# Performance work log

Measured on AMD Instinct MI355X. Metric: run time of the kernel, lower is better.

Reference implementation:

```python
import jax, jax.numpy as jnp
import numpy as np


def dequantize_sparse_sinq(W_q, scales, zeros, mask, scale2, group_size):
    """SINQ-style dual-scaled grouped dequant with sparsity mask.

    W = ((W_q - zeros) * scales) broadcast over groups along the in-dim,
    then scaled per input column by scale2, then masked (pruned weights -> 0).
    W_q: [O, I] int; scales/zeros: [O, I//g]; scale2: [I]; mask: [O, I] bool.
    """
    O, I = W_q.shape
    g = group_size
    Wq = W_q.astype(jnp.float32).reshape(O, I // g, g)
    W = (Wq - zeros[:, :, None]) * scales[:, :, None]  # grouped affine dequant
    W = W.reshape(O, I) * scale2[None, :]              # second (column) scale
    return jnp.where(mask, W, jnp.zeros((), dtype=W.dtype))


def setup_inputs() -> dict:
    key = jax.random.key(0)
    ks = jax.random.split(key, 7)
    B, S, I, O, G = 8, 2048, 4096, 4096, 128
    x = jax.random.normal(ks[0], (B, S, I), dtype=jnp.float32)
    W_q = jax.random.randint(ks[1], (O, I), 0, 16, dtype=jnp.int32)
    scales = jax.random.uniform(ks[2], (O, I // G), dtype=jnp.float32)
    zeros = jax.random.uniform(ks[3], (O, I // G), dtype=jnp.float32)
    mask = jax.random.randint(ks[4], (O, I), 0, 2, dtype=jnp.int32).astype(jnp.bool_)
    scale2 = jax.random.uniform(ks[5], (I,), dtype=jnp.float32)
    bias = jax.random.normal(ks[6], (O,), dtype=jnp.float32)
    return {"x": x, "W_q": W_q, "scales": scales, "zeros": zeros,
            "mask": mask, "scale2": scale2, "bias": bias, "group_size": G}


def reference(x, W_q, scales, zeros, mask, scale2, bias, group_size):
    W = dequantize_sparse_sinq(W_q, scales, zeros, mask, scale2, group_size)
    W = W.astype(x.dtype)
    out = jnp.einsum('bsi,oi->bso', x, W)  # matmul(x, W.T)
    out = out + bias
    return out
```

## Files before the change

### kernel.cpp

```cpp
#include <hip/hip_runtime.h>
#include <hip/hip_bf16.h>
#include <stdint.h>


typedef short s16x8 __attribute__((ext_vector_type(8)));
typedef short s16x4 __attribute__((ext_vector_type(4)));
typedef float f32x4 __attribute__((ext_vector_type(4)));

#define BM 128
#define BN 128
#define BK 64
#define LDSS 72

static __device__ __forceinline__ short f2bf(float f) {
    __hip_bfloat16 h = __float2bfloat16(f);
    return *reinterpret_cast<short*>(&h);
}

__global__ __launch_bounds__(256)
void dequant_kernel(const int* __restrict__ Wq,
                    const float* __restrict__ scales,
                    const float* __restrict__ zeros,
                    const void* __restrict__ mask_raw,
                    const float* __restrict__ scale2,
                    short* __restrict__ Wb,
                    int O, int I, int G) {
    __shared__ int lds_flag;
    if (threadIdx.x == 0) lds_flag = 0;
    __syncthreads();
    {
        unsigned v = ((const unsigned*)mask_raw)[threadIdx.x & 255];
        if (v > 1u) lds_flag = 1;
    }
    __syncthreads();
    const bool mask_is_byte = (lds_flag != 0);

    long long idx = ((long long)blockIdx.x * 256 + threadIdx.x) * 8;
    if (idx >= (long long)O * I) return;
    int o = (int)(idx / I);
    int i = (int)(idx % I);
    int gi = o * (I / G) + i / G;
    float s = scales[gi];
    float z = zeros[gi];

    int4 w0 = *(const int4*)(Wq + idx);
    int4 w1 = *(const int4*)(Wq + idx + 4);
    float4 s2a = *(const float4*)(scale2 + i);
    float4 s2b = *(const float4*)(scale2 + i + 4);

    unsigned m[8];
    if (mask_is_byte) {
        unsigned long long mb = *(const unsigned long long*)((const unsigned char*)mask_raw + idx);
        #pragma unroll
        for (int j = 0; j < 8; ++j) m[j] = (unsigned)((mb >> (8 * j)) & 0xffULL);
    } else {
        int4 ma = *(const int4*)((const int*)mask_raw + idx);
        int4 mbv = *(const int4*)((const int*)mask_raw + idx + 4);
        m[0] = ma.x;  m[1] = ma.y;  m[2] = ma.z;  m[3] = ma.w;
        m[4] = mbv.x; m[5] = mbv.y; m[6] = mbv.z; m[7] = mbv.w;
    }

    float v[8];
    v[0] = ((float)w0.x - z) * s * s2a.x;
    v[1] = ((float)w0.y - z) * s * s2a.y;
    v[2] = ((float)w0.z - z) * s * s2a.z;
    v[3] = ((float)w0.w - z) * s * s2a.w;
    v[4] = ((float)w1.x - z) * s * s2b.x;
    v[5] = ((float)w1.y - z) * s * s2b.y;
    v[6] = ((float)w1.z - z) * s * s2b.z;
    v[7] = ((float)w1.w - z) * s * s2b.w;

    union { s16x8 v; int4 q; } out;
    #pragma unroll
    for (int j = 0; j < 8; ++j) {
        float masked = m[j] ? v[j] : 0.0f;
        out.v[j] = f2bf(masked);
    }
    *(int4*)(Wb + idx) = out.q;
}

__global__ __launch_bounds__(256, 2)
void gemm_kernel(const float* __restrict__ X,
                 const short* __restrict__ Wb,
                 const float* __restrict__ bias,
                 float* __restrict__ Out,
                 int M, int N, int K) {
    __shared__ short As[BM * LDSS];
    __shared__ short Bs[BN * LDSS];

    const int tid  = threadIdx.x;
    const int m0   = blockIdx.y * BM;
    const int n0   = blockIdx.x * BN;
    const int wave = tid >> 6;
    const int lane = tid & 63;
    const int wm   = (wave >> 1) * 64;
    const int wn   = (wave & 1) * 64;
    const int lr   = lane & 15;
    const int lq   = lane >> 4;

    f32x4 acc[4][4] = {};

    for (int k0 = 0; k0 < K; k0 += BK) {
        #pragma unroll
        for (int t = 0; t < 8; ++t) {
            int c   = tid + t * 256;
            int row = c >> 4;
            int col = (c & 15) * 4;
            float4 xv = *(const float4*)(X + (size_t)(m0 + row) * K + k0 + col);
            s16x4 bv;
            bv[0] = f2bf(xv.x); bv[1] = f2bf(xv.y);
            bv[2] = f2bf(xv.z); bv[3] = f2bf(xv.w);
            *(s16x4*)&As[row * LDSS + col] = bv;
        }
        #pragma unroll
        for (int t = 0; t < 4; ++t) {
            int c   = tid + t * 256;
            int row = c >> 3;
            int col = (c & 7) * 8;
            s16x8 wv = *(const s16x8*)(Wb + (size_t)(n0 + row) * K + k0 + col);
            *(s16x8*)&Bs[row * LDSS + col] = wv;
        }
        __syncthreads();

        #pragma unroll
        for (int kk = 0; kk < BK; kk += 32) {
            s16x8 af[4], bf[4];
            #pragma unroll
            for (int mi = 0; mi < 4; ++mi)
                af[mi] = *(const s16x8*)&As[(wm + mi * 16 + lr) * LDSS + kk + lq * 8];
            #pragma unroll
            for (int ni = 0; ni < 4; ++ni)
                bf[ni] = *(const s16x8*)&Bs[(wn + ni * 16 + lr) * LDSS + kk + lq * 8];
            #pragma unroll
            for (int mi = 0; mi < 4; ++mi)
                #pragma unroll
                for (int ni = 0; ni < 4; ++ni)
                    acc[mi][ni] = __builtin_amdgcn_mfma_f32_16x16x32_bf16(
                        af[mi], bf[ni], acc[mi][ni], 0, 0, 0);
        }
        __syncthreads();
    }

    #pragma unroll
    for (int ni = 0; ni < 4; ++ni) {
        int nc = n0 + wn + ni * 16 + lr;
        float bv = bias[nc];
        #pragma unroll
        for (int mi = 0; mi < 4; ++mi) {
            int mr = m0 + wm + mi * 16 + lq * 4;
            #pragma unroll
            for (int r = 0; r < 4; ++r)
                Out[(size_t)(mr + r) * N + nc] = acc[mi][ni][r] + bv;
        }
    }
}

extern "C" void kernel_launch(void* const* d_in, const int* in_sizes, int n_in,
                              void* d_out, int out_size, void* d_ws, size_t ws_size,
                              hipStream_t stream) {
    const float* x      = (const float*)d_in[0];
    const int*   Wq     = (const int*)d_in[1];
    const float* scales = (const float*)d_in[2];
    const float* zeros  = (const float*)d_in[3];
    const void*  mask   = (const void*)d_in[4];
    const float* scale2 = (const float*)d_in[5];
    const float* bias   = (const float*)d_in[6];
    float*       out    = (float*)d_out;

    const int I = in_sizes[5];
    const int O = in_sizes[6];
    const int M = (int)(in_sizes[0] / I);
    const int G = (int)(((long long)O * I) / in_sizes[2]);

    short* Wb = (short*)d_ws;

    long long total = (long long)O * I;
    int dq_blocks = (int)((total / 8 + 255) / 256);
    dequant_kernel<<<dq_blocks, 256, 0, stream>>>(Wq, scales, zeros, mask,
                                                  scale2, Wb, O, I, G);

    dim3 grid(O / BN, M / BM);
    gemm_kernel<<<grid, 256, 0, stream>>>(x, Wb, bias, out, M, O, I);
}
```

Before: 1.161 ms.

## Pre-convert activations to bf16 and stream GEMM tiles directly into LDS

Adds a separate kernel that converts X from fp32 to bf16 in workspace. A new GEMM then loads both bf16 operands straight from global memory into LDS with global_load_lds, avoiding per-tile conversion and register staging. It also switches the dequant indexing to 32-bit arithmetic. The cost is an extra full pass over X: an fp32 read plus a bf16 write. The unpadded 64-wide LDS rows may also cause bank conflicts during fragment reads. The new path runs only when the workspace is large enough.

```diff
diff --git a/kernel.cpp b/kernel.cpp
--- a/kernel.cpp
+++ b/kernel.cpp
@@ -35,10 +35,10 @@
     __syncthreads();
     const bool mask_is_byte = (lds_flag != 0);
 
-    long long idx = ((long long)blockIdx.x * 256 + threadIdx.x) * 8;
-    if (idx >= (long long)O * I) return;
-    int o = (int)(idx / I);
-    int i = (int)(idx % I);
+    int idx = (blockIdx.x * 256 + threadIdx.x) * 8;
+    if (idx >= O * I) return;
+    int o = idx / I;
+    int i = idx - o * I;
     int gi = o * (I / G) + i / G;
     float s = scales[gi];
     float z = zeros[gi];
@@ -77,6 +77,90 @@
         out.v[j] = f2bf(masked);
     }
     *(int4*)(Wb + idx) = out.q;
+}
+
+__global__ __launch_bounds__(256)
+void convert_x_kernel(const float* __restrict__ X, short* __restrict__ Xb, int n8) {
+    int c = blockIdx.x * 256 + threadIdx.x;
+    if (c >= n8) return;
+    size_t idx = (size_t)c * 8;
+    float4 a = *(const float4*)(X + idx);
+    float4 b = *(const float4*)(X + idx + 4);
+    union { s16x8 v; int4 q; } o;
+    o.v[0] = f2bf(a.x); o.v[1] = f2bf(a.y); o.v[2] = f2bf(a.z); o.v[3] = f2bf(a.w);
+    o.v[4] = f2bf(b.x); o.v[5] = f2bf(b.y); o.v[6] = f2bf(b.z); o.v[7] = f2bf(b.w);
+    *(int4*)(Xb + idx) = o.q;
+}
+
+__global__ __launch_bounds__(256, 2)
+void gemm_bb_kernel(const short* __restrict__ Xb,
+                    const short* __restrict__ Wb,
+                    const float* __restrict__ bias,
+                    float* __restrict__ Out,
+                    int M, int N, int K) {
+    __shared__ short As[BM * BK];
+    __shared__ short Bs[BN * BK];
+
+    const int tid  = threadIdx.x;
+    const int m0   = blockIdx.y * BM;
+    const int n0   = blockIdx.x * BN;
+    const int wave = tid >> 6;
+    const int lane = tid & 63;
+    const int wm   = (wave >> 1) * 64;
+    const int wn   = (wave & 1) * 64;
+    const int lr   = lane & 15;
+    const int lq   = lane >> 4;
+
+    f32x4 acc[4][4] = {};
+
+    const short* gA = Xb + (size_t)(m0 + (tid >> 3)) * K + (tid & 7) * 8;
+    const short* gB = Wb + (size_t)(n0 + (tid >> 3)) * K + (tid & 7) * 8;
+    short* lA = &As[wave * 512];
+    short* lB = &Bs[wave * 512];
+
+    for (int k0 = 0; k0 < K; k0 += BK) {
+        #pragma unroll
+        for (int t = 0; t < 4; ++t) {
+            __builtin_amdgcn_global_load_lds(
+                (const __attribute__((address_space(1))) void*)(gA + (size_t)t * 32 * K + k0),
+                (__attribute__((address_space(3))) void*)(lA + t * 2048), 16, 0, 0);
+            __builtin_amdgcn_global_load_lds(
+                (const __attribute__((address_space(1))) void*)(gB + (size_t)t * 32 * K + k0),
+                (__attribute__((address_space(3))) void*)(lB + t * 2048), 16, 0, 0);
+        }
+        __syncthreads();
+
+        #pragma unroll
+        for (int kk = 0; kk < BK; kk += 32) {
+            s16x8 af[4], bfv[4];
+            #pragma unroll
+            for (int mi = 0; mi < 4; ++mi)
+                af[mi] = *(const s16x8*)&As[(wm + mi * 16 + lr) * BK + kk + lq * 8];
+            #pragma unroll
+            for (int ni = 0; ni < 4; ++ni)
+                bfv[ni] = *(const s16x8*)&Bs[(wn + ni * 16 + lr) * BK + kk + lq * 8];
+            #pragma unroll
+            for (int mi = 0; mi < 4; ++mi)
+                #pragma unroll
+                for (int ni = 0; ni < 4; ++ni)
+                    acc[mi][ni] = __builtin_amdgcn_mfma_f32_16x16x32_bf16(
+                        af[mi], bfv[ni], acc[mi][ni], 0, 0, 0);
+        }
+        __syncthreads();
+    }
+
+    #pragma unroll
+    for (int ni = 0; ni < 4; ++ni) {
+        int nc = n0 + wn + ni * 16 + lr;
+        float bv = bias[nc];
+        #pragma unroll
+        for (int mi = 0; mi < 4; ++mi) {
+            int mr = m0 + wm + mi * 16 + lq * 4;
+            #pragma unroll
+            for (int r = 0; r < 4; ++r)
+                Out[(size_t)(mr + r) * N + nc] = acc[mi][ni][r] + bv;
+        }
+    }
 }
 
 __global__ __launch_bounds__(256, 2)
@@ -173,12 +257,22 @@
     const int G = (int)(((long long)O * I) / in_sizes[2]);
 
     short* Wb = (short*)d_ws;
-
-    long long total = (long long)O * I;
-    int dq_blocks = (int)((total / 8 + 255) / 256);
+    size_t wbBytes = (size_t)O * I * sizeof(short);
+    size_t xbBytes = (size_t)M * I * sizeof(short);
+
+    long long totalW = (long long)O * I;
+    int dq_blocks = (int)((totalW / 8 + 255) / 256);
     dequant_kernel<<<dq_blocks, 256, 0, stream>>>(Wq, scales, zeros, mask,
                                                   scale2, Wb, O, I, G);
 
     dim3 grid(O / BN, M / BM);
-    gemm_kernel<<<grid, 256, 0, stream>>>(x, Wb, bias, out, M, O, I);
-}
+    if (ws_size >= wbBytes + xbBytes) {
+        short* Xb = (short*)((char*)d_ws + wbBytes);
+        int n8 = (int)(((size_t)M * I) / 8);
+        int cv_blocks = (n8 + 255) / 256;
+        convert_x_kernel<<<cv_blocks, 256, 0, stream>>>(x, Xb, n8);
+        gemm_bb_kernel<<<grid, 256, 0, stream>>>(Xb, Wb, bias, out, M, O, I);
+    } else {
+        gemm_kernel<<<grid, 256, 0, stream>>>(x, Wb, bias, out, M, O, I);
+    }
+}
```

Result: no change. 1.142 ms (-1.7%).
